# Optimization experiments

Measured on AMD Instinct MI355X. Metric: run time of the kernel, lower is better.

## Reference

```python
import jax, jax.numpy as jnp
import numpy as np
from jax import lax


def _conv2d(x, w, b, stride):
    # x: [B,C,H,W], w: [O,I,kh,kw], b: [O]
    y = lax.conv_general_dilated(
        x, w, window_strides=(stride, stride), padding='VALID',
        dimension_numbers=('NCHW', 'OIHW', 'NCHW'))
    return y + b[None, :, None, None]


def setup_inputs() -> dict:
    key = jax.random.key(0)
    ks = jax.random.split(key, 4)
    B, C, H, W = 8, 128, 128, 128
    x = jax.random.normal(ks[0], (B, C, H, W), dtype=jnp.float32)
    # conv weights, scaled like torch default init (~1/sqrt(fan_in))
    Wq = jax.random.normal(ks[1], (C, C, 2, 2), dtype=jnp.float32) / np.sqrt(C * 4)
    Wk = jax.random.normal(ks[2], (C, C, 2, 2), dtype=jnp.float32) / np.sqrt(C * 4)
    Wv = jax.random.normal(ks[3], (C, C, 1, 1), dtype=jnp.float32) / np.sqrt(C)
    bq = jnp.zeros((C,), dtype=jnp.float32)
    bk = jnp.zeros((C,), dtype=jnp.float32)
    bv = jnp.zeros((C,), dtype=jnp.float32)
    return {'x': x, 'Wq': Wq, 'bq': bq, 'Wk': Wk, 'bk': bk, 'Wv': Wv, 'bv': bv}


def reference(x, Wq, bq, Wk, bk, Wv, bv):
    B, C, H, W = x.shape
    # query/key: 2x2 stride-2 convs -> [B, C, (H//2)*(W//2)]
    q = _conv2d(x, Wq, bq, 2).reshape(B, C, -1)
    k = _conv2d(x, Wk, bk, 2).reshape(B, C, -1)
    # value: 1x1 conv -> [B, C, H*W]
    v = _conv2d(x, Wv, bv, 1).reshape(B, C, -1)
    # energy: [B, C, C]
    energy = jnp.einsum('bcn,bdn->bcd', q, k)
    # max-subtract trick: softmax over (row_max - energy)
    energy_new = jnp.max(energy, axis=-1, keepdims=True) - energy
    attention = jax.nn.softmax(energy_new, axis=-1)
    out = jnp.einsum('bcd,bdn->bcn', attention, v)
    return out.reshape(B, C, H, W)
```

## Files before the change

### kernel.cpp

```cpp
#include <hip/hip_runtime.h>
#include <math.h>


typedef float f32x4 __attribute__((ext_vector_type(4)));
typedef short s16x8 __attribute__((ext_vector_type(8)));

__device__ __forceinline__ unsigned short f2bf(float f) {
  union { float f; unsigned u; } v; v.f = f;
  unsigned r = v.u + 0x7FFFu + ((v.u >> 16) & 1u);
  return (unsigned short)(r >> 16);
}
__device__ __forceinline__ float bf2f(unsigned short h) {
  union { unsigned u; float f; } v; v.u = ((unsigned)h) << 16;
  return v.f;
}
__device__ __forceinline__ unsigned pack2(unsigned short a, unsigned short b) {
  return (unsigned)a | ((unsigned)b << 16);
}

__global__ __launch_bounds__(256) void k_prep(
    const float* __restrict__ Wq, const float* __restrict__ Wk,
    unsigned short* __restrict__ Wth, unsigned short* __restrict__ Wtl) {
  const int f = (blockIdx.x * 256 + threadIdx.x) * 4;
  const int row = f >> 9;
  const int k   = f & 511;
  const float* src = (row < 128) ? &Wq[row * 512 + k] : &Wk[(row - 128) * 512 + k];
  float4 v = *(const float4*)src;
  unsigned short h0 = f2bf(v.x), h1 = f2bf(v.y), h2 = f2bf(v.z), h3 = f2bf(v.w);
  unsigned short l0 = f2bf(v.x - bf2f(h0)), l1 = f2bf(v.y - bf2f(h1));
  unsigned short l2 = f2bf(v.z - bf2f(h2)), l3 = f2bf(v.w - bf2f(h3));
  const int di = (k >> 5) * 8192 + row * 32 + (k & 31);
  *(ushort4*)&Wth[di] = make_ushort4(h0, h1, h2, h3);
  *(ushort4*)&Wtl[di] = make_ushort4(l0, l1, l2, l3);
}

__global__ __launch_bounds__(256, 2) void k_conv_energy(
    const float* __restrict__ x,
    const unsigned short* __restrict__ Wth, const unsigned short* __restrict__ Wtl,
    const float* __restrict__ bq, const float* __restrict__ bk,
    float* __restrict__ epart) {
  __shared__ unsigned short LDS[32768];
  unsigned short* Th = LDS;
  unsigned short* Tl = LDS + 16384;

  const int t = threadIdx.x;
  const int nt = blockIdx.x, b = blockIdx.y;
  const int w = t >> 6, lane = t & 63;
  const int lrow = lane & 15, lkb = lane >> 4;

  const int pp = t >> 4;
  const int ci_l = pp >> 1, kh = pp & 1;
  const int i16 = t & 15;
  const int klb = ci_l * 4 + kh * 2;
  const float* xb = x + ((size_t)b << 21);
  const float* xrow = xb + (size_t)ci_l * 16384 + (2 * nt + kh) * 128 + 2 * i16;

  f32x4 acc[4][4];
#pragma unroll
  for (int m = 0; m < 4; ++m)
#pragma unroll
    for (int n = 0; n < 4; ++n) acc[m][n] = (f32x4){0.f, 0.f, 0.f, 0.f};

  s16x8 pfh[2][4], pfl[2][4];
  s16x8 bfh[2][4], bfl[2][4];
  float2 pv[2][4];
  const int aoff = (w * 64 + lrow) * 32 + lkb * 8;

#pragma unroll
  for (int m = 0; m < 4; ++m) {
    pfh[0][m] = *(const s16x8*)&Wth[aoff + m * 512];
    pfl[0][m] = *(const s16x8*)&Wtl[aoff + m * 512];
    pfh[1][m] = *(const s16x8*)&Wth[8192 + aoff + m * 512];
    pfl[1][m] = *(const s16x8*)&Wtl[8192 + aoff + m * 512];
  }
#pragma unroll
  for (int g = 0; g < 4; ++g) pv[1][g] = *(const float2*)&xrow[32 * g];
  {
    unsigned short* Nh = LDS;
    unsigned short* Nl = LDS + 2560;
#pragma unroll
    for (int g = 0; g < 4; ++g) {
      const int n = i16 + 16 * g;
      unsigned short hx = f2bf(pv[1][g].x), hy = f2bf(pv[1][g].y);
      *(unsigned*)&Nh[n * 40 + klb] = pack2(hx, hy);
      *(unsigned*)&Nl[n * 40 + klb] = pack2(f2bf(pv[1][g].x - bf2f(hx)),
                                            f2bf(pv[1][g].y - bf2f(hy)));
    }
  }
#pragma unroll
  for (int g = 0; g < 4; ++g)
    pv[1][g] = *(const float2*)&xrow[(size_t)8 * 16384 + 32 * g];
  __syncthreads();
#pragma unroll
  for (int nf = 0; nf < 4; ++nf) {
    const int bidx = (nf * 16 + lrow) * 40 + lkb * 8;
    bfh[0][nf] = *(const s16x8*)&LDS[bidx];
    bfl[0][nf] = *(const s16x8*)&LDS[2560 + bidx];
  }

#pragma unroll
  for (int step = 0; step < 16; ++step) {
    const int cur = step & 1;
    if (step < 15) {
      unsigned short* Nh = LDS + (cur ^ 1) * 5120;
      unsigned short* Nl = Nh + 2560;
#pragma unroll
      for (int g = 0; g < 4; ++g) {
        const int n = i16 + 16 * g;
        unsigned short hx = f2bf(pv[cur ^ 1][g].x), hy = f2bf(pv[cur ^ 1][g].y);
        *(unsigned*)&Nh[n * 40 + klb] = pack2(hx, hy);
        *(unsigned*)&Nl[n * 40 + klb] = pack2(f2bf(pv[cur ^ 1][g].x - bf2f(hx)),
                                              f2bf(pv[cur ^ 1][g].y - bf2f(hy)));
      }
      asm volatile("s_waitcnt lgkmcnt(0)" ::: "memory");
      __builtin_amdgcn_s_barrier();
      const unsigned short* Bh = LDS + (cur ^ 1) * 5120;
      const unsigned short* Bl = Bh + 2560;
#pragma unroll
      for (int nf = 0; nf < 4; ++nf) {
        const int bidx = (nf * 16 + lrow) * 40 + lkb * 8;
        bfh[cur ^ 1][nf] = *(const s16x8*)&Bh[bidx];
        bfl[cur ^ 1][nf] = *(const s16x8*)&Bl[bidx];
      }
    }
    if (step < 14) {
#pragma unroll
      for (int g = 0; g < 4; ++g)
        pv[cur][g] = *(const float2*)&xrow[(size_t)(step + 2) * 8 * 16384 + 32 * g];
    }
#pragma unroll
    for (int m = 0; m < 4; ++m)
#pragma unroll
      for (int n = 0; n < 4; ++n) {
        acc[m][n] = __builtin_amdgcn_mfma_f32_16x16x32_bf16(pfh[cur][m], bfh[cur][n], acc[m][n], 0, 0, 0);
        acc[m][n] = __builtin_amdgcn_mfma_f32_16x16x32_bf16(pfh[cur][m], bfl[cur][n], acc[m][n], 0, 0, 0);
        acc[m][n] = __builtin_amdgcn_mfma_f32_16x16x32_bf16(pfl[cur][m], bfh[cur][n], acc[m][n], 0, 0, 0);
      }
    if (step < 14) {
      const unsigned short* Wh_n = Wth + (step + 2) * 8192;
      const unsigned short* Wl_n = Wtl + (step + 2) * 8192;
#pragma unroll
      for (int m = 0; m < 4; ++m) {
        pfh[cur][m] = *(const s16x8*)&Wh_n[aoff + m * 512];
        pfl[cur][m] = *(const s16x8*)&Wl_n[aoff + m * 512];
      }
    }
  }
  __syncthreads();

  const float* biasp = (w < 2) ? bq : bk;
  const int rb = (w & 1) * 64;
  float biasr[16];
#pragma unroll
  for (int m = 0; m < 4; ++m)
#pragma unroll
    for (int i = 0; i < 4; ++i)
      biasr[m * 4 + i] = biasp[rb + m * 16 + (lane >> 4) * 4 + i];

#pragma unroll
  for (int m = 0; m < 4; ++m) {
    const int r0 = w * 64 + m * 16 + (lane >> 4) * 4;
#pragma unroll
    for (int n = 0; n < 4; ++n) {
      const int c = n * 16 + lrow;
      const int c8 = c >> 3, c7 = c & 7;
#pragma unroll
      for (int i = 0; i < 4; ++i) {
        const int r = r0 + i;
        const float vv = acc[m][n][i] + biasr[m * 4 + i];
        const unsigned short h = f2bf(vv);
        const unsigned short l = f2bf(vv - bf2f(h));
        const int ad = r * 64 + (((c8 ^ (r & 7))) << 3) + c7;
        Th[ad] = h;
        Tl[ad] = l;
      }
    }
  }
  __syncthreads();

  f32x4 e[4][4];
#pragma unroll
  for (int m = 0; m < 4; ++m)
#pragma unroll
    for (int n = 0; n < 4; ++n) e[m][n] = (f32x4){0.f, 0.f, 0.f, 0.f};

  const int mrow0 = (w >> 1) * 64;
  const int nrow0 = 128 + (w & 1) * 64;
#pragma unroll
  for (int ks = 0; ks < 2; ++ks) {
    const int c8 = ks * 4 + lkb;
    s16x8 qh[4], ql[4], kh8[4], kl8[4];
#pragma unroll
    for (int m = 0; m < 4; ++m) {
      const int r = mrow0 + m * 16 + lrow;
      const int ad = r * 64 + ((c8 ^ (r & 7)) << 3);
      qh[m] = *(const s16x8*)&Th[ad];
      ql[m] = *(const s16x8*)&Tl[ad];
    }
#pragma unroll
    for (int n = 0; n < 4; ++n) {
      const int r = nrow0 + n * 16 + lrow;
      const int ad = r * 64 + ((c8 ^ (r & 7)) << 3);
      kh8[n] = *(const s16x8*)&Th[ad];
      kl8[n] = *(const s16x8*)&Tl[ad];
    }
#pragma unroll
    for (int m = 0; m < 4; ++m)
#pragma unroll
      for (int n = 0; n < 4; ++n) {
        e[m][n] = __builtin_amdgcn_mfma_f32_16x16x32_bf16(qh[m], kh8[n], e[m][n], 0, 0, 0);
        e[m][n] = __builtin_amdgcn_mfma_f32_16x16x32_bf16(qh[m], kl8[n], e[m][n], 0, 0, 0);
        e[m][n] = __builtin_amdgcn_mfma_f32_16x16x32_bf16(ql[m], kh8[n], e[m][n], 0, 0, 0);
      }
  }
  float* ep = epart + ((size_t)b * 64 + nt) * 16384;
#pragma unroll
  for (int m = 0; m < 4; ++m) {
    const int qr = (w >> 1) * 64 + m * 16 + (lane >> 4) * 4;
#pragma unroll
    for (int n = 0; n < 4; ++n) {
      const int kr = (w & 1) * 64 + n * 16 + lrow;
#pragma unroll
      for (int i = 0; i < 4; ++i) ep[(size_t)(qr + i) * 128 + kr] = e[m][n][i];
    }
  }
}

__global__ __launch_bounds__(256) void k_softmax_M(
    const float* __restrict__ epart, const float* __restrict__ Wv,
    const float* __restrict__ bv, float* __restrict__ Mbuf,
    float* __restrict__ outbb) {
  __shared__ float As[4][2][128];
  const int t = threadIdx.x;
  const int wid = t >> 6, lane = t & 63;
  const int half = lane >> 5, l32 = lane & 31;
  const int b = blockIdx.x >> 4;
  const int c = (blockIdx.x & 15) * 8 + wid * 2 + half;
  const int d0 = l32 * 4;

  float4 s = make_float4(0.f, 0.f, 0.f, 0.f);
#pragma unroll 8
  for (int p = 0; p < 64; ++p) {
    float4 e = *(const float4*)&epart[((size_t)b * 64 + p) * 16384 + c * 128 + d0];
    s.x += e.x; s.y += e.y; s.z += e.z; s.w += e.w;
  }
  float mn = fminf(fminf(s.x, s.y), fminf(s.z, s.w));
#pragma unroll
  for (int off = 1; off < 32; off <<= 1) mn = fminf(mn, __shfl_xor(mn, off));
  const float p0 = expf(mn - s.x);
  const float p1 = expf(mn - s.y);
  const float p2 = expf(mn - s.z);
  const float p3 = expf(mn - s.w);
  float tot = (p0 + p1) + (p2 + p3);
#pragma unroll
  for (int off = 1; off < 32; off <<= 1) tot += __shfl_xor(tot, off);
  const float inv = 1.f / tot;
  const float a0 = p0 * inv, a1 = p1 * inv, a2 = p2 * inv, a3 = p3 * inv;

  const float4 bvv = *(const float4*)&bv[d0];
  float ob = a0 * bvv.x + a1 * bvv.y + a2 * bvv.z + a3 * bvv.w;
#pragma unroll
  for (int off = 1; off < 32; off <<= 1) ob += __shfl_xor(ob, off);
  if (l32 == 0) outbb[b * 128 + c] = ob;

  *(float4*)&As[wid][half][d0] = make_float4(a0, a1, a2, a3);
  float4 m = make_float4(0.f, 0.f, 0.f, 0.f);
#pragma unroll 4
  for (int d = 0; d < 128; ++d) {
    const float a = As[wid][half][d];
    const float4 wv = *(const float4*)&Wv[d * 128 + d0];
    m.x = fmaf(a, wv.x, m.x);
    m.y = fmaf(a, wv.y, m.y);
    m.z = fmaf(a, wv.z, m.z);
    m.w = fmaf(a, wv.w, m.w);
  }
  *(float4*)&Mbuf[(size_t)b * 16384 + c * 128 + d0] = m;
}

__global__ __launch_bounds__(256) void k_out(
    const float* __restrict__ x, const float* __restrict__ Mbuf,
    const float* __restrict__ outbb, float* __restrict__ out) {
  __shared__ unsigned short Ms[128 * 40];
  __shared__ unsigned short Xs[128 * 40];
  const int t = threadIdx.x;
  const int nt = blockIdx.x, b = blockIdx.y;
  const int wid = t >> 6, lane = t & 63;
  const int wr = wid >> 1, wc = wid & 1;
  const int lrow = lane & 15, lkb = lane >> 4;
  const int am = t >> 1, ak0 = (t & 1) * 16;
  const int xkl = (t >> 5) * 4;
  const int xc0 = (t & 31) * 4;

  const float* xb = x + ((size_t)b << 21);
  const float* Mb = Mbuf + (size_t)b * 16384;
  float* ob = out + ((size_t)b << 21);

  f32x4 acc[4][4];
#pragma unroll
  for (int m = 0; m < 4; ++m)
#pragma unroll
    for (int n = 0; n < 4; ++n) acc[m][n] = (f32x4){0.f, 0.f, 0.f, 0.f};

  for (int step = 0; step < 4; ++step) {
    const int kk = step * 32;
    {
      float w[16];
      *(float4*)&w[0]  = *(const float4*)&Mb[am * 128 + kk + ak0];
      *(float4*)&w[4]  = *(const float4*)&Mb[am * 128 + kk + ak0 + 4];
      *(float4*)&w[8]  = *(const float4*)&Mb[am * 128 + kk + ak0 + 8];
      *(float4*)&w[12] = *(const float4*)&Mb[am * 128 + kk + ak0 + 12];
      unsigned short hs[16];
#pragma unroll
      for (int i = 0; i < 16; ++i) hs[i] = f2bf(w[i]);
      *(uint4*)&Ms[am * 40 + ak0]     = *(uint4*)&hs[0];
      *(uint4*)&Ms[am * 40 + ak0 + 8] = *(uint4*)&hs[8];
    }
#pragma unroll
    for (int q = 0; q < 4; ++q) {
      const int kl = xkl + q;
      float4 v = *(const float4*)&xb[(size_t)(kk + kl) * 16384 + nt * 128 + xc0];
      Xs[(xc0 + 0) * 40 + kl] = f2bf(v.x);
      Xs[(xc0 + 1) * 40 + kl] = f2bf(v.y);
      Xs[(xc0 + 2) * 40 + kl] = f2bf(v.z);
      Xs[(xc0 + 3) * 40 + kl] = f2bf(v.w);
    }
    __syncthreads();
    s16x8 af[4], bf[4];
#pragma unroll
    for (int m = 0; m < 4; ++m)
      af[m] = *(const s16x8*)&Ms[(wr * 64 + m * 16 + lrow) * 40 + lkb * 8];
#pragma unroll
    for (int n = 0; n < 4; ++n)
      bf[n] = *(const s16x8*)&Xs[(wc * 64 + n * 16 + lrow) * 40 + lkb * 8];
#pragma unroll
    for (int m = 0; m < 4; ++m)
#pragma unroll
      for (int n = 0; n < 4; ++n)
        acc[m][n] = __builtin_amdgcn_mfma_f32_16x16x32_bf16(af[m], bf[n], acc[m][n], 0, 0, 0);
    __syncthreads();
  }
#pragma unroll
  for (int m = 0; m < 4; ++m) {
    const int r0 = wr * 64 + m * 16 + (lane >> 4) * 4;
#pragma unroll
    for (int n = 0; n < 4; ++n) {
      const int gc = nt * 128 + wc * 64 + n * 16 + (lane & 15);
#pragma unroll
      for (int i = 0; i < 4; ++i) {
        const int row = r0 + i;
        ob[(size_t)row * 16384 + gc] = acc[m][n][i] + outbb[b * 128 + row];
      }
    }
  }
}

extern "C" void kernel_launch(void* const* d_in, const int* in_sizes, int n_in,
                              void* d_out, int out_size, void* d_ws, size_t ws_size,
                              hipStream_t stream) {
  const float* x  = (const float*)d_in[0];
  const float* Wq = (const float*)d_in[1];
  const float* bq = (const float*)d_in[2];
  const float* Wk = (const float*)d_in[3];
  const float* bk = (const float*)d_in[4];
  const float* Wv = (const float*)d_in[5];
  const float* bv = (const float*)d_in[6];
  float* out = (float*)d_out;
  char* ws = (char*)d_ws;

  float* epart = (float*)ws;
  float* Mbuf  = (float*)(ws + 33554432);
  float* outbb = (float*)(ws + 34078720);
  unsigned short* Wth = (unsigned short*)(ws + 34082816);
  unsigned short* Wtl = (unsigned short*)(ws + 34344960);

  hipLaunchKernelGGL(k_prep, dim3(128), dim3(256), 0, stream, Wq, Wk, Wth, Wtl);
  hipLaunchKernelGGL(k_conv_energy, dim3(64, 8), dim3(256), 0, stream,
                     x, Wth, Wtl, bq, bk, epart);
  hipLaunchKernelGGL(k_softmax_M, dim3(128), dim3(256), 0, stream,
                     epart, Wv, bv, Mbuf, outbb);
  hipLaunchKernelGGL(k_out, dim3(128, 8), dim3(256), 0, stream,
                     x, Mbuf, outbb, out);
}
```

Baseline: 85.85 us.

## Halve conv-energy LDS and drop register double buffers to raise occupancy

The conv+energy kernel now stages the Q/K tile through LDS in two 32-column halves, which halves shared memory to 32 KB. The weight-fragment and B-fragment register double buffers become single buffers, with B fragments read from LDS right before the MFMAs and weights prefetched one step ahead instead of two. Launch bounds rise from 2 to 3 blocks per CU to make use of the freed LDS and registers. The cost is less latency hiding inside each wave and an extra barrier in the energy phase.

```diff
diff --git a/kernel.cpp b/kernel.cpp
--- a/kernel.cpp
+++ b/kernel.cpp
@@ -34,14 +34,14 @@
   *(ushort4*)&Wtl[di] = make_ushort4(l0, l1, l2, l3);
 }
 
-__global__ __launch_bounds__(256, 2) void k_conv_energy(
+__global__ __launch_bounds__(256, 3) void k_conv_energy(
     const float* __restrict__ x,
     const unsigned short* __restrict__ Wth, const unsigned short* __restrict__ Wtl,
     const float* __restrict__ bq, const float* __restrict__ bk,
     float* __restrict__ epart) {
-  __shared__ unsigned short LDS[32768];
+  __shared__ unsigned short LDS[16384];
   unsigned short* Th = LDS;
-  unsigned short* Tl = LDS + 16384;
+  unsigned short* Tl = LDS + 8192;
 
   const int t = threadIdx.x;
   const int nt = blockIdx.x, b = blockIdx.y;
@@ -61,46 +61,73 @@
 #pragma unroll
     for (int n = 0; n < 4; ++n) acc[m][n] = (f32x4){0.f, 0.f, 0.f, 0.f};
 
-  s16x8 pfh[2][4], pfl[2][4];
-  s16x8 bfh[2][4], bfl[2][4];
+  s16x8 pfh[4], pfl[4];
   float2 pv[2][4];
   const int aoff = (w * 64 + lrow) * 32 + lkb * 8;
 
 #pragma unroll
   for (int m = 0; m < 4; ++m) {
-    pfh[0][m] = *(const s16x8*)&Wth[aoff + m * 512];
-    pfl[0][m] = *(const s16x8*)&Wtl[aoff + m * 512];
-    pfh[1][m] = *(const s16x8*)&Wth[8192 + aoff + m * 512];
-    pfl[1][m] = *(const s16x8*)&Wtl[8192 + aoff + m * 512];
-  }
-#pragma unroll
-  for (int g = 0; g < 4; ++g) pv[1][g] = *(const float2*)&xrow[32 * g];
+    pfh[m] = *(const s16x8*)&Wth[aoff + m * 512];
+    pfl[m] = *(const s16x8*)&Wtl[aoff + m * 512];
+  }
   {
-    unsigned short* Nh = LDS;
-    unsigned short* Nl = LDS + 2560;
-#pragma unroll
-    for (int g = 0; g < 4; ++g) {
-      const int n = i16 + 16 * g;
-      unsigned short hx = f2bf(pv[1][g].x), hy = f2bf(pv[1][g].y);
-      *(unsigned*)&Nh[n * 40 + klb] = pack2(hx, hy);
-      *(unsigned*)&Nl[n * 40 + klb] = pack2(f2bf(pv[1][g].x - bf2f(hx)),
-                                            f2bf(pv[1][g].y - bf2f(hy)));
-    }
+    float2 v0 = *(const float2*)&xrow[0];
+    float2 v1 = *(const float2*)&xrow[32];
+    float2 v2 = *(const float2*)&xrow[64];
+    float2 v3 = *(const float2*)&xrow[96];
+    unsigned short hx, hy;
+    hx = f2bf(v0.x); hy = f2bf(v0.y);
+    *(unsigned*)&LDS[(i16     ) * 40 + klb] = pack2(hx, hy);
+    *(unsigned*)&LDS[2560 + (i16     ) * 40 + klb] = pack2(f2bf(v0.x - bf2f(hx)), f2bf(v0.y - bf2f(hy)));
+    hx = f2bf(v1.x); hy = f2bf(v1.y);
+    *(unsigned*)&LDS[(i16 + 16) * 40 + klb] = pack2(hx, hy);
+    *(unsigned*)&LDS[2560 + (i16 + 16) * 40 + klb] = pack2(f2bf(v1.x - bf2f(hx)), f2bf(v1.y - bf2f(hy)));
+    hx = f2bf(v2.x); hy = f2bf(v2.y);
+    *(unsigned*)&LDS[(i16 + 32) * 40 + klb] = pack2(hx, hy);
+    *(unsigned*)&LDS[2560 + (i16 + 32) * 40 + klb] = pack2(f2bf(v2.x - bf2f(hx)), f2bf(v2.y - bf2f(hy)));
+    hx = f2bf(v3.x); hy = f2bf(v3.y);
+    *(unsigned*)&LDS[(i16 + 48) * 40 + klb] = pack2(hx, hy);
+    *(unsigned*)&LDS[2560 + (i16 + 48) * 40 + klb] = pack2(f2bf(v3.x - bf2f(hx)), f2bf(v3.y - bf2f(hy)));
   }
 #pragma unroll
   for (int g = 0; g < 4; ++g)
     pv[1][g] = *(const float2*)&xrow[(size_t)8 * 16384 + 32 * g];
   __syncthreads();
-#pragma unroll
-  for (int nf = 0; nf < 4; ++nf) {
-    const int bidx = (nf * 16 + lrow) * 40 + lkb * 8;
-    bfh[0][nf] = *(const s16x8*)&LDS[bidx];
-    bfl[0][nf] = *(const s16x8*)&LDS[2560 + bidx];
-  }
 
 #pragma unroll
   for (int step = 0; step < 16; ++step) {
     const int cur = step & 1;
+    const unsigned short* Bh = LDS + cur * 5120;
+    const unsigned short* Bl = Bh + 2560;
+    s16x8 bfh[4], bfl[4];
+#pragma unroll
+    for (int nf = 0; nf < 4; ++nf) {
+      const int bidx = (nf * 16 + lrow) * 40 + lkb * 8;
+      bfh[nf] = *(const s16x8*)&Bh[bidx];
+      bfl[nf] = *(const s16x8*)&Bl[bidx];
+    }
+#pragma unroll
+    for (int m = 0; m < 4; ++m)
+#pragma unroll
+      for (int n = 0; n < 4; ++n) {
+        acc[m][n] = __builtin_amdgcn_mfma_f32_16x16x32_bf16(pfh[m], bfh[n], acc[m][n], 0, 0, 0);
+        acc[m][n] = __builtin_amdgcn_mfma_f32_16x16x32_bf16(pfh[m], bfl[n], acc[m][n], 0, 0, 0);
+        acc[m][n] = __builtin_amdgcn_mfma_f32_16x16x32_bf16(pfl[m], bfh[n], acc[m][n], 0, 0, 0);
+      }
+    if (step < 15) {
+      const unsigned short* Wh_n = Wth + (step + 1) * 8192;
+      const unsigned short* Wl_n = Wtl + (step + 1) * 8192;
+#pragma unroll
+      for (int m = 0; m < 4; ++m) {
+        pfh[m] = *(const s16x8*)&Wh_n[aoff + m * 512];
+        pfl[m] = *(const s16x8*)&Wl_n[aoff + m * 512];
+      }
+    }
+    if (step < 14) {
+#pragma unroll
+      for (int g = 0; g < 4; ++g)
+        pv[cur][g] = *(const float2*)&xrow[(size_t)(step + 2) * 8 * 16384 + 32 * g];
+    }
     if (step < 15) {
       unsigned short* Nh = LDS + (cur ^ 1) * 5120;
       unsigned short* Nl = Nh + 2560;
@@ -114,36 +141,6 @@
       }
       asm volatile("s_waitcnt lgkmcnt(0)" ::: "memory");
       __builtin_amdgcn_s_barrier();
-      const unsigned short* Bh = LDS + (cur ^ 1) * 5120;
-      const unsigned short* Bl = Bh + 2560;
-#pragma unroll
-      for (int nf = 0; nf < 4; ++nf) {
-        const int bidx = (nf * 16 + lrow) * 40 + lkb * 8;
-        bfh[cur ^ 1][nf] = *(const s16x8*)&Bh[bidx];
-        bfl[cur ^ 1][nf] = *(const s16x8*)&Bl[bidx];
-      }
-    }
-    if (step < 14) {
-#pragma unroll
-      for (int g = 0; g < 4; ++g)
-        pv[cur][g] = *(const float2*)&xrow[(size_t)(step + 2) * 8 * 16384 + 32 * g];
-    }
-#pragma unroll
-    for (int m = 0; m < 4; ++m)
-#pragma unroll
-      for (int n = 0; n < 4; ++n) {
-        acc[m][n] = __builtin_amdgcn_mfma_f32_16x16x32_bf16(pfh[cur][m], bfh[cur][n], acc[m][n], 0, 0, 0);
-        acc[m][n] = __builtin_amdgcn_mfma_f32_16x16x32_bf16(pfh[cur][m], bfl[cur][n], acc[m][n], 0, 0, 0);
-        acc[m][n] = __builtin_amdgcn_mfma_f32_16x16x32_bf16(pfl[cur][m], bfh[cur][n], acc[m][n], 0, 0, 0);
-      }
-    if (step < 14) {
-      const unsigned short* Wh_n = Wth + (step + 2) * 8192;
-      const unsigned short* Wl_n = Wtl + (step + 2) * 8192;
-#pragma unroll
-      for (int m = 0; m < 4; ++m) {
-        pfh[cur][m] = *(const s16x8*)&Wh_n[aoff + m * 512];
-        pfl[cur][m] = *(const s16x8*)&Wl_n[aoff + m * 512];
-      }
     }
   }
   __syncthreads();
@@ -157,27 +154,6 @@
     for (int i = 0; i < 4; ++i)
       biasr[m * 4 + i] = biasp[rb + m * 16 + (lane >> 4) * 4 + i];
 
-#pragma unroll
-  for (int m = 0; m < 4; ++m) {
-    const int r0 = w * 64 + m * 16 + (lane >> 4) * 4;
-#pragma unroll
-    for (int n = 0; n < 4; ++n) {
-      const int c = n * 16 + lrow;
-      const int c8 = c >> 3, c7 = c & 7;
-#pragma unroll
-      for (int i = 0; i < 4; ++i) {
-        const int r = r0 + i;
-        const float vv = acc[m][n][i] + biasr[m * 4 + i];
-        const unsigned short h = f2bf(vv);
-        const unsigned short l = f2bf(vv - bf2f(h));
-        const int ad = r * 64 + (((c8 ^ (r & 7))) << 3) + c7;
-        Th[ad] = h;
-        Tl[ad] = l;
-      }
-    }
-  }
-  __syncthreads();
-
   f32x4 e[4][4];
 #pragma unroll
   for (int m = 0; m < 4; ++m)
@@ -186,33 +162,58 @@
 
   const int mrow0 = (w >> 1) * 64;
   const int nrow0 = 128 + (w & 1) * 64;
+
 #pragma unroll
   for (int ks = 0; ks < 2; ++ks) {
-    const int c8 = ks * 4 + lkb;
-    s16x8 qh[4], ql[4], kh8[4], kl8[4];
 #pragma unroll
     for (int m = 0; m < 4; ++m) {
-      const int r = mrow0 + m * 16 + lrow;
-      const int ad = r * 64 + ((c8 ^ (r & 7)) << 3);
-      qh[m] = *(const s16x8*)&Th[ad];
-      ql[m] = *(const s16x8*)&Tl[ad];
-    }
-#pragma unroll
-    for (int n = 0; n < 4; ++n) {
-      const int r = nrow0 + n * 16 + lrow;
-      const int ad = r * 64 + ((c8 ^ (r & 7)) << 3);
-      kh8[n] = *(const s16x8*)&Th[ad];
-      kl8[n] = *(const s16x8*)&Tl[ad];
-    }
-#pragma unroll
-    for (int m = 0; m < 4; ++m)
+      const int r0 = w * 64 + m * 16 + (lane >> 4) * 4;
+#pragma unroll
+      for (int nn = 0; nn < 2; ++nn) {
+        const int n = 2 * ks + nn;
+        const int cl = nn * 16 + lrow;
+        const int cl8 = cl >> 3, c7 = cl & 7;
+#pragma unroll
+        for (int i = 0; i < 4; ++i) {
+          const int r = r0 + i;
+          const float vv = acc[m][n][i] + biasr[m * 4 + i];
+          const unsigned short h = f2bf(vv);
+          const unsigned short l = f2bf(vv - bf2f(h));
+          const int ad = r * 32 + ((cl8 ^ (r & 3)) << 3) + c7;
+          Th[ad] = h;
+          Tl[ad] = l;
+        }
+      }
+    }
+    __syncthreads();
+    {
+      s16x8 qh[4], ql[4], kh8[4], kl8[4];
+#pragma unroll
+      for (int m = 0; m < 4; ++m) {
+        const int r = mrow0 + m * 16 + lrow;
+        const int ad = r * 32 + ((lkb ^ (r & 3)) << 3);
+        qh[m] = *(const s16x8*)&Th[ad];
+        ql[m] = *(const s16x8*)&Tl[ad];
+      }
 #pragma unroll
       for (int n = 0; n < 4; ++n) {
-        e[m][n] = __builtin_amdgcn_mfma_f32_16x16x32_bf16(qh[m], kh8[n], e[m][n], 0, 0, 0);
-        e[m][n] = __builtin_amdgcn_mfma_f32_16x16x32_bf16(qh[m], kl8[n], e[m][n], 0, 0, 0);
-        e[m][n] = __builtin_amdgcn_mfma_f32_16x16x32_bf16(ql[m], kh8[n], e[m][n], 0, 0, 0);
-      }
-  }
+        const int r = nrow0 + n * 16 + lrow;
+        const int ad = r * 32 + ((lkb ^ (r & 3)) << 3);
+        kh8[n] = *(const s16x8*)&Th[ad];
+        kl8[n] = *(const s16x8*)&Tl[ad];
+      }
+#pragma unroll
+      for (int m = 0; m < 4; ++m)
+#pragma unroll
+        for (int n = 0; n < 4; ++n) {
+          e[m][n] = __builtin_amdgcn_mfma_f32_16x16x32_bf16(qh[m], kh8[n], e[m][n], 0, 0, 0);
+          e[m][n] = __builtin_amdgcn_mfma_f32_16x16x32_bf16(qh[m], kl8[n], e[m][n], 0, 0, 0);
+          e[m][n] = __builtin_amdgcn_mfma_f32_16x16x32_bf16(ql[m], kh8[n], e[m][n], 0, 0, 0);
+        }
+    }
+    if (ks == 0) __syncthreads();
+  }
+
   float* ep = epart + ((size_t)b * 64 + nt) * 16384;
 #pragma unroll
   for (int m = 0; m < 4; ++m) {
```

New measurement: 84.23 us. About the same (-1.9%).
